# Optimization experiments

Measured on AMD Instinct MI355X. Metric: run time of the kernel, lower is better.

## Reference

```python
import jax, jax.numpy as jnp
import numpy as np

B = 8192          # num_envs
OPT = 16          # num options
SHARED = 22       # shared_state_size (hardcoded in module)
UNIQ = 8          # unique_state_size (hardcoded in module)
MIN_DUR, MAX_DUR = 0.1, 0.5  # const.gait_net.valid_swing_duration_range


def _w(k, o, i):
    return jax.random.normal(k, (o, i), jnp.float32) * (1.0 / np.sqrt(i))


def setup_inputs() -> dict:
    key = jax.random.key(0)
    ks = jax.random.split(key, 20)
    obs = jax.random.normal(ks[0], (B, SHARED + OPT * UNIQ), jnp.float32)
    flag = jax.random.uniform(ks[1], (B, OPT)) < 0.25
    u = obs[:, SHARED:].reshape(B, OPT, UNIQ)
    u = u.at[:, :, 0].set(jnp.where(flag, 1.0, u[:, :, 0]))
    obs = jnp.concatenate([obs[:, :SHARED], u.reshape(B, OPT * UNIQ)], axis=1)
    return {
        "obs": obs,
        "sw1": _w(ks[2], 256, 22), "sb1": jnp.zeros((256,), jnp.float32),
        "sw2": _w(ks[3], 256, 256), "sb2": jnp.zeros((256,), jnp.float32),
        "uw1": _w(ks[4], 128, 8), "ub1": jnp.zeros((128,), jnp.float32),
        "uw2": _w(ks[5], 128, 128), "ub2": jnp.zeros((128,), jnp.float32),
        "no_op_embedding": jax.random.normal(ks[6], (128,), jnp.float32),
        "tw1": _w(ks[7], 512, 384), "tb1": jnp.zeros((512,), jnp.float32),
        "tw2": _w(ks[8], 256, 512), "tb2": jnp.zeros((256,), jnp.float32),
        "vw": _w(ks[9], 1, 256), "vb": jnp.zeros((1,), jnp.float32),
        "dw": _w(ks[10], 1, 256), "db": jnp.zeros((1,), jnp.float32),
    }


def reference(obs, sw1, sb1, sw2, sb2, uw1, ub1, uw2, ub2, no_op_embedding,
              tw1, tb1, tw2, tb2, vw, vb, dw, db):
    relu = jax.nn.relu
    shared = obs[:, :SHARED]                               # [B, 22]
    uniq = obs[:, SHARED:].reshape(B, OPT, UNIQ)           # [B, OPT, 8]
    # shared encoder (22 -> 256 -> 256, relu output)
    se = relu(relu(shared @ sw1.T + sb1) @ sw2.T + sb2)    # [B, 256]
    # unique encoder applied to all options at once (8 -> 128 -> 128)
    ue = relu(relu(uniq @ uw1.T + ub1) @ uw2.T + ub2)      # [B, OPT, 128]
    no_op = uniq[:, :, 0] == 1.0                           # [B, OPT]
    ue = jnp.where(no_op[..., None], no_op_embedding, ue)
    trunk_in = jnp.concatenate(
        [jnp.broadcast_to(se[:, None, :], (B, OPT, se.shape[-1])), ue], axis=-1)
    t = relu(relu(trunk_in @ tw1.T + tb1) @ tw2.T + tb2)   # [B, OPT, 256]
    logits = (t @ vw.T + vb).squeeze(-1)                   # [B, OPT]
    duration = jax.nn.sigmoid((t @ dw.T + db).squeeze(-1)) * (MAX_DUR - MIN_DUR) + MIN_DUR
    return logits, duration
```

## Files before the change

kernel.cpp:

```cpp
#include <hip/hip_runtime.h>
#include <stdint.h>


static constexpr int B_ = 8192;

typedef __attribute__((ext_vector_type(8))) short bf16x8;
typedef __attribute__((ext_vector_type(4))) float f32x4;

__device__ __forceinline__ float u2f(uint16_t u) {
    union { uint32_t i; float f; } c; c.i = (uint32_t)u << 16; return c.f;
}
__device__ __forceinline__ uint16_t f2u(float f) {
    union { float f; uint32_t i; } c; c.f = f;
    uint32_t x = c.i;
    return (uint16_t)((x + 0x7FFFu + ((x >> 16) & 1u)) >> 16);
}

static constexpr size_t WCSE   = 0;
static constexpr size_t WTW1SE = 4194304;
static constexpr size_t WTW1UE = WTW1SE + 131072;
static constexpr size_t WTW2   = WTW1UE + 65536;
static constexpr size_t WUW2   = WTW2 + 131072;
static constexpr size_t WSW2   = WUW2 + 16384;
static constexpr size_t WUW1B  = WSW2 + 65536;

__global__ __launch_bounds__(256) void k_conv(
    const float* __restrict__ tw1, const float* __restrict__ tw2,
    const float* __restrict__ uw2, const float* __restrict__ sw2,
    const float* __restrict__ uw1, uint16_t* __restrict__ ws)
{
    int i4 = blockIdx.x * 256 + threadIdx.x;
    if (i4 >= 102400) {
        int q = i4 - 102400;
        int n = q >> 3, k0 = (q & 7) * 4;
        ushort4 o = {0, 0, 0, 0};
        if (k0 < 8) {
            float4 v = *reinterpret_cast<const float4*>(uw1 + n * 8 + k0);
            o.x = f2u(v.x); o.y = f2u(v.y); o.z = f2u(v.z); o.w = f2u(v.w);
        }
        *reinterpret_cast<ushort4*>(ws + WUW1B + n * 32 + k0) = o;
        return;
    }
    const float* src; size_t dst;
    if (i4 < 32768) {
        int g = i4 * 4, n = g >> 8, k = g & 255;
        src = tw1 + (size_t)n * 384 + k;
        dst = WTW1SE + (size_t)g;
    } else if (i4 < 49152) {
        int q = i4 - 32768, n = q >> 5, w = q & 31;
        src = tw1 + (size_t)n * 384 + 256 + w * 4;
        dst = WTW1UE + (size_t)n * 128 + w * 4;
    } else if (i4 < 81920) {
        int q = (i4 - 49152) * 4;
        src = tw2 + q; dst = WTW2 + q;
    } else if (i4 < 86016) {
        int q = (i4 - 81920) * 4;
        src = uw2 + q; dst = WUW2 + q;
    } else {
        int q = (i4 - 86016) * 4;
        src = sw2 + q; dst = WSW2 + q;
    }
    float4 v = *reinterpret_cast<const float4*>(src);
    ushort4 o;
    o.x = f2u(v.x); o.y = f2u(v.y); o.z = f2u(v.z); o.w = f2u(v.w);
    *reinterpret_cast<ushort4*>(ws + dst) = o;
}

__global__ __launch_bounds__(512) void k_cse(
    const float* __restrict__ obs,
    const float* __restrict__ sw1, const float* __restrict__ sb1,
    const float* __restrict__ sb2, const float* __restrict__ tb1,
    uint16_t* __restrict__ ws)
{
    __shared__ float xs[16][24];
    __shared__ uint16_t h1s[16 * 264];
    __shared__ uint16_t seL[16 * 264];
    const int t = threadIdx.x;
    const int b0 = blockIdx.x * 16;
    const uint16_t* sw2b   = ws + WSW2;
    const uint16_t* tw1seb = ws + WTW1SE;

    if (t < 352) {
        int e = t / 22, c = t - e * 22;
        xs[e][c] = obs[(size_t)(b0 + e) * 150 + c];
    }
    __syncthreads();
    {
        const int n = t & 255;
        float w[22];
        #pragma unroll
        for (int k = 0; k < 22; ++k) w[k] = sw1[n * 22 + k];
        const float bias = sb1[n];
        #pragma unroll
        for (int ii = 0; ii < 8; ++ii) {
            int e = (t >> 8) * 8 + ii;
            float a = bias;
            #pragma unroll
            for (int k = 0; k < 22; ++k) a += w[k] * xs[e][k];
            h1s[e * 264 + n] = f2u(fmaxf(a, 0.f));
        }
    }
    __syncthreads();
    const int wv = t >> 6, lane = t & 63, quad = lane >> 4, l16 = lane & 15;
    {
        f32x4 acc[2];
        #pragma unroll
        for (int nt = 0; nt < 2; ++nt) {
            float bv = sb2[wv * 32 + nt * 16 + l16];
            acc[nt] = {bv, bv, bv, bv};
        }
        const uint16_t* bb = sw2b + (size_t)(wv * 32 + l16) * 256 + quad * 8;
        bf16x8 bc[2], bn[2];
        bc[0] = *reinterpret_cast<const bf16x8*>(bb);
        bc[1] = *reinterpret_cast<const bf16x8*>(bb + 4096);
        #pragma unroll
        for (int kk = 0; kk < 8; ++kk) {
            if (kk < 7) {
                bn[0] = *reinterpret_cast<const bf16x8*>(bb + (kk + 1) * 32);
                bn[1] = *reinterpret_cast<const bf16x8*>(bb + 4096 + (kk + 1) * 32);
            }
            bf16x8 af = *reinterpret_cast<const bf16x8*>(
                &h1s[l16 * 264 + kk * 32 + quad * 8]);
            #pragma unroll
            for (int nt = 0; nt < 2; ++nt)
                acc[nt] = __builtin_amdgcn_mfma_f32_16x16x32_bf16(
                    af, bc[nt], acc[nt], 0, 0, 0);
            bc[0] = bn[0]; bc[1] = bn[1];
        }
        #pragma unroll
        for (int nt = 0; nt < 2; ++nt)
            #pragma unroll
            for (int r = 0; r < 4; ++r)
                seL[(quad * 4 + r) * 264 + wv * 32 + nt * 16 + l16] =
                    f2u(fmaxf(acc[nt][r], 0.f));
    }
    __syncthreads();
    {
        f32x4 acc[4];
        #pragma unroll
        for (int nt = 0; nt < 4; ++nt) {
            float bv = tb1[wv * 64 + nt * 16 + l16];
            acc[nt] = {bv, bv, bv, bv};
        }
        const uint16_t* bb = tw1seb + (size_t)(wv * 64 + l16) * 256 + quad * 8;
        bf16x8 bc[4], bn[4];
        #pragma unroll
        for (int nt = 0; nt < 4; ++nt)
            bc[nt] = *reinterpret_cast<const bf16x8*>(bb + nt * 4096);
        #pragma unroll
        for (int kk = 0; kk < 8; ++kk) {
            if (kk < 7) {
                #pragma unroll
                for (int nt = 0; nt < 4; ++nt)
                    bn[nt] = *reinterpret_cast<const bf16x8*>(
                        bb + nt * 4096 + (kk + 1) * 32);
            }
            bf16x8 af = *reinterpret_cast<const bf16x8*>(
                &seL[l16 * 264 + kk * 32 + quad * 8]);
            #pragma unroll
            for (int nt = 0; nt < 4; ++nt)
                acc[nt] = __builtin_amdgcn_mfma_f32_16x16x32_bf16(
                    af, bc[nt], acc[nt], 0, 0, 0);
            #pragma unroll
            for (int nt = 0; nt < 4; ++nt) bc[nt] = bn[nt];
        }
        #pragma unroll
        for (int nt = 0; nt < 4; ++nt)
            #pragma unroll
            for (int r = 0; r < 4; ++r)
                ws[WCSE + (size_t)(b0 + quad * 4 + r) * 512 +
                   wv * 64 + nt * 16 + l16] = f2u(acc[nt][r]);
    }
}

static constexpr int UQB_OFF  = 0;
static constexpr int NOOP_OFF = 5120;
static constexpr int CSE_OFF  = 5376;
static constexpr int H1U_OFF  = 9472;
static constexpr int UET_OFF  = 26880;
static constexpr int H1T_OFF  = 44288;
static constexpr int SMEM_SZ  = 78080;

__global__ __launch_bounds__(512, 4) void k_main(
    const float* __restrict__ obs,
    const float* __restrict__ ub1,
    const float* __restrict__ ub2, const float* __restrict__ emb,
    const float* __restrict__ tb2,
    const float* __restrict__ vw,  const float* __restrict__ vb,
    const float* __restrict__ dw,  const float* __restrict__ db,
    const uint16_t* __restrict__ wsb,
    float* __restrict__ out)
{
    __shared__ __align__(16) char smem[SMEM_SZ];
    uint16_t* uqb   = (uint16_t*)(smem + UQB_OFF);
    float*    noopf = (float*)(smem + NOOP_OFF);
    uint16_t* cseL  = (uint16_t*)(smem + CSE_OFF);
    uint16_t* h1u   = (uint16_t*)(smem + H1U_OFF);
    uint16_t* uet   = (uint16_t*)(smem + UET_OFF);
    uint16_t* h1t   = (uint16_t*)(smem + H1T_OFF);
    uint16_t* t2    = h1t;

    const int t    = threadIdx.x;
    const int wv   = t >> 6;
    const int lane = t & 63;
    const int quad = lane >> 4;
    const int l16  = lane & 15;
    const int b0   = blockIdx.x * 4;

    const uint16_t* csep  = wsb + WCSE;
    const uint16_t* tw1ue = wsb + WTW1UE;
    const uint16_t* tw2b  = wsb + WTW2;
    const uint16_t* uw2b  = wsb + WUW2;
    const uint16_t* uw1b  = wsb + WUW1B;

    {
        int r = t >> 3, q = t & 7;
        int e = r >> 4, o = r & 15;
        ushort4 ov = {0, 0, 0, 0};
        if (q < 2) {
            const float2* sp = reinterpret_cast<const float2*>(
                &obs[(size_t)(b0 + e) * 150 + 22 + o * 8 + q * 4]);
            float2 a = sp[0], b = sp[1];
            ov.x = f2u(a.x); ov.y = f2u(a.y); ov.z = f2u(b.x); ov.w = f2u(b.y);
        }
        *reinterpret_cast<ushort4*>(&uqb[r * 40 + q * 4]) = ov;
        #pragma unroll
        for (int ii = 0; ii < 2; ++ii) {
            int i = t + ii * 512;
            int ee = i >> 8, cc = i & 255;
            ((uint32_t*)cseL)[ee * 256 + cc] =
                ((const uint32_t*)(csep + (size_t)(b0 + ee) * 512))[cc];
        }
        if (t < 64) {
            int ee = t >> 4, oo = t & 15;
            noopf[t] = (obs[(size_t)(b0 + ee) * 150 + 22 + oo * 8] == 1.0f) ? 1.0f : 0.0f;
        }
    }
    __syncthreads();

    {
        const int n = wv * 16 + l16;
        const float bv = ub1[n];
        f32x4 acc[4];
        #pragma unroll
        for (int mt = 0; mt < 4; ++mt) acc[mt] = {bv, bv, bv, bv};
        bf16x8 bf = *reinterpret_cast<const bf16x8*>(&uw1b[n * 32 + quad * 8]);
        #pragma unroll
        for (int mt = 0; mt < 4; ++mt) {
            bf16x8 af = *reinterpret_cast<const bf16x8*>(
                &uqb[(mt * 16 + l16) * 40 + quad * 8]);
            acc[mt] = __builtin_amdgcn_mfma_f32_16x16x32_bf16(af, bf, acc[mt], 0, 0, 0);
        }
        #pragma unroll
        for (int mt = 0; mt < 4; ++mt)
            #pragma unroll
            for (int r = 0; r < 4; ++r) {
                int row = mt * 16 + quad * 4 + r;
                h1u[row * 136 + n] = f2u(fmaxf(acc[mt][r], 0.f));
            }
    }
    __syncthreads();

    {
        const int n = wv * 16 + l16;
        const float bv = ub2[n];
        const float ev = emb[n];
        f32x4 acc[4];
        #pragma unroll
        for (int mt = 0; mt < 4; ++mt) acc[mt] = {bv, bv, bv, bv};
        #pragma unroll
        for (int kk = 0; kk < 4; ++kk) {
            bf16x8 bf = *reinterpret_cast<const bf16x8*>(
                &uw2b[(size_t)n * 128 + kk * 32 + quad * 8]);
            #pragma unroll
            for (int mt = 0; mt < 4; ++mt) {
                bf16x8 af = *reinterpret_cast<const bf16x8*>(
                    &h1u[(mt * 16 + l16) * 136 + kk * 32 + quad * 8]);
                acc[mt] = __builtin_amdgcn_mfma_f32_16x16x32_bf16(af, bf, acc[mt], 0, 0, 0);
            }
        }
        #pragma unroll
        for (int mt = 0; mt < 4; ++mt)
            #pragma unroll
            for (int r = 0; r < 4; ++r) {
                int row = mt * 16 + quad * 4 + r;
                float v = (noopf[row] != 0.0f) ? ev : fmaxf(acc[mt][r], 0.f);
                uet[row * 136 + n] = f2u(v);
            }
    }
    __syncthreads();

    f32x4 acc2[4][2];
    #pragma unroll
    for (int nt = 0; nt < 2; ++nt) {
        float bv = tb2[wv * 32 + nt * 16 + l16];
        #pragma unroll
        for (int mt = 0; mt < 4; ++mt) acc2[mt][nt] = {bv, bv, bv, bv};
    }

    #pragma unroll
    for (int nc = 0; nc < 2; ++nc) {
        {
            f32x4 acc1[4][2];
            #pragma unroll
            for (int nt = 0; nt < 2; ++nt) {
                int n = nc * 256 + wv * 32 + nt * 16 + l16;
                #pragma unroll
                for (int mt = 0; mt < 4; ++mt) {
                    float v = u2f(cseL[mt * 512 + n]);
                    acc1[mt][nt] = {v, v, v, v};
                }
            }
            const uint16_t* bb = tw1ue + (size_t)(nc * 256 + wv * 32 + l16) * 128
                                 + quad * 8;
            bf16x8 bc[2], bn[2];
            bc[0] = *reinterpret_cast<const bf16x8*>(bb);
            bc[1] = *reinterpret_cast<const bf16x8*>(bb + 2048);
            #pragma unroll
            for (int kk = 0; kk < 4; ++kk) {
                if (kk < 3) {
                    bn[0] = *reinterpret_cast<const bf16x8*>(bb + (kk + 1) * 32);
                    bn[1] = *reinterpret_cast<const bf16x8*>(bb + 2048 + (kk + 1) * 32);
                }
                bf16x8 af[4];
                #pragma unroll
                for (int mt = 0; mt < 4; ++mt)
                    af[mt] = *reinterpret_cast<const bf16x8*>(
                        &uet[(mt * 16 + l16) * 136 + kk * 32 + quad * 8]);
                #pragma unroll
                for (int mt = 0; mt < 4; ++mt)
                    #pragma unroll
                    for (int nt = 0; nt < 2; ++nt)
                        acc1[mt][nt] = __builtin_amdgcn_mfma_f32_16x16x32_bf16(
                            af[mt], bc[nt], acc1[mt][nt], 0, 0, 0);
                bc[0] = bn[0]; bc[1] = bn[1];
            }
            #pragma unroll
            for (int mt = 0; mt < 4; ++mt)
                #pragma unroll
                for (int nt = 0; nt < 2; ++nt)
                    #pragma unroll
                    for (int r = 0; r < 4; ++r) {
                        int row = mt * 16 + quad * 4 + r;
                        h1t[row * 264 + wv * 32 + nt * 16 + l16] =
                            f2u(fmaxf(acc1[mt][nt][r], 0.f));
                    }
        }
        __syncthreads();
        {
            const uint16_t* cb = tw2b + (size_t)(wv * 32 + l16) * 512 + nc * 256
                                 + quad * 8;
            bf16x8 cc[2], cn[2];
            cc[0] = *reinterpret_cast<const bf16x8*>(cb);
            cc[1] = *reinterpret_cast<const bf16x8*>(cb + 8192);
            #pragma unroll
            for (int k2 = 0; k2 < 8; ++k2) {
                if (k2 < 7) {
                    cn[0] = *reinterpret_cast<const bf16x8*>(cb + (k2 + 1) * 32);
                    cn[1] = *reinterpret_cast<const bf16x8*>(cb + 8192 + (k2 + 1) * 32);
                }
                bf16x8 af[4];
                #pragma unroll
                for (int mt = 0; mt < 4; ++mt)
                    af[mt] = *reinterpret_cast<const bf16x8*>(
                        &h1t[(mt * 16 + l16) * 264 + k2 * 32 + quad * 8]);
                #pragma unroll
                for (int mt = 0; mt < 4; ++mt)
                    #pragma unroll
                    for (int nt = 0; nt < 2; ++nt)
                        acc2[mt][nt] = __builtin_amdgcn_mfma_f32_16x16x32_bf16(
                            af[mt], cc[nt], acc2[mt][nt], 0, 0, 0);
                cc[0] = cn[0]; cc[1] = cn[1];
            }
        }
        if (nc == 0) __syncthreads();
    }
    __syncthreads();
    #pragma unroll
    for (int mt = 0; mt < 4; ++mt)
        #pragma unroll
        for (int nt = 0; nt < 2; ++nt)
            #pragma unroll
            for (int r = 0; r < 4; ++r) {
                int row = mt * 16 + quad * 4 + r;
                t2[row * 264 + wv * 32 + nt * 16 + l16] =
                    f2u(fmaxf(acc2[mt][nt][r], 0.f));
            }
    __syncthreads();

    {
        float vwf[4], dwf[4];
        #pragma unroll
        for (int j = 0; j < 4; ++j) {
            vwf[j] = vw[lane + 64 * j];
            dwf[j] = dw[lane + 64 * j];
        }
        const float vbf = vb[0], dbf = db[0];
        #pragma unroll
        for (int rr = 0; rr < 8; ++rr) {
            int row = wv * 8 + rr;
            float sv = 0.f, sd = 0.f;
            #pragma unroll
            for (int j = 0; j < 4; ++j) {
                float tv = u2f(t2[row * 264 + lane + 64 * j]);
                sv += tv * vwf[j];
                sd += tv * dwf[j];
            }
            #pragma unroll
            for (int off = 32; off > 0; off >>= 1) {
                sv += __shfl_down(sv, off);
                sd += __shfl_down(sd, off);
            }
            if (lane == 0) {
                int g = blockIdx.x * 64 + row;
                out[g] = sv + vbf;
                float z = sd + dbf;
                float sig = 1.f / (1.f + __expf(-z));
                out[B_ * 16 + g] = sig * 0.4f + 0.1f;
            }
        }
    }
}

extern "C" void kernel_launch(void* const* d_in, const int* in_sizes, int n_in,
                              void* d_out, int out_size, void* d_ws, size_t ws_size,
                              hipStream_t stream) {
    const float* obs = (const float*)d_in[0];
    const float* sw1 = (const float*)d_in[1];
    const float* sb1 = (const float*)d_in[2];
    const float* sw2 = (const float*)d_in[3];
    const float* sb2 = (const float*)d_in[4];
    const float* uw1 = (const float*)d_in[5];
    const float* ub1 = (const float*)d_in[6];
    const float* uw2 = (const float*)d_in[7];
    const float* ub2 = (const float*)d_in[8];
    const float* emb = (const float*)d_in[9];
    const float* tw1 = (const float*)d_in[10];
    const float* tb1 = (const float*)d_in[11];
    const float* tw2 = (const float*)d_in[12];
    const float* tb2 = (const float*)d_in[13];
    const float* vw  = (const float*)d_in[14];
    const float* vb  = (const float*)d_in[15];
    const float* dw  = (const float*)d_in[16];
    const float* db  = (const float*)d_in[17];

    uint16_t* wsb = (uint16_t*)d_ws;

    k_conv<<<404, 256, 0, stream>>>(tw1, tw2, uw2, sw2, uw1, wsb);
    k_cse<<<512, 512, 0, stream>>>(obs, sw1, sb1, sb2, tb1, wsb);
    k_main<<<B_ / 4, 512, 0, stream>>>(obs, ub1, ub2, emb, tb2,
                                       vw, vb, dw, db, wsb, (float*)d_out);
}
```

Baseline: 239.3 us.

## Fuse shared-encoder kernel into main kernel, keep per-env trunk contribution in LDS

Removes the separate k_cse launch. Each k_main block now computes the shared encoder (22->256->256) and its tw1 contribution for its own 4 environments, writing the result straight into LDS instead of round-tripping a 512-wide bf16 vector per env through global workspace. This saves one kernel launch and the global write/read of the precomputed shared contribution. The cost is that the MFMA tiles use 16 rows where only 4 are valid, so most of that shared-encoder compute is wasted, and every block reloads the sw2/tw1se weights.

```diff
diff --git a/kernel.cpp b/kernel.cpp
--- a/kernel.cpp
+++ b/kernel.cpp
@@ -66,123 +66,21 @@
     *reinterpret_cast<ushort4*>(ws + dst) = o;
 }
 
-__global__ __launch_bounds__(512) void k_cse(
-    const float* __restrict__ obs,
-    const float* __restrict__ sw1, const float* __restrict__ sb1,
-    const float* __restrict__ sb2, const float* __restrict__ tb1,
-    uint16_t* __restrict__ ws)
-{
-    __shared__ float xs[16][24];
-    __shared__ uint16_t h1s[16 * 264];
-    __shared__ uint16_t seL[16 * 264];
-    const int t = threadIdx.x;
-    const int b0 = blockIdx.x * 16;
-    const uint16_t* sw2b   = ws + WSW2;
-    const uint16_t* tw1seb = ws + WTW1SE;
-
-    if (t < 352) {
-        int e = t / 22, c = t - e * 22;
-        xs[e][c] = obs[(size_t)(b0 + e) * 150 + c];
-    }
-    __syncthreads();
-    {
-        const int n = t & 255;
-        float w[22];
-        #pragma unroll
-        for (int k = 0; k < 22; ++k) w[k] = sw1[n * 22 + k];
-        const float bias = sb1[n];
-        #pragma unroll
-        for (int ii = 0; ii < 8; ++ii) {
-            int e = (t >> 8) * 8 + ii;
-            float a = bias;
-            #pragma unroll
-            for (int k = 0; k < 22; ++k) a += w[k] * xs[e][k];
-            h1s[e * 264 + n] = f2u(fmaxf(a, 0.f));
-        }
-    }
-    __syncthreads();
-    const int wv = t >> 6, lane = t & 63, quad = lane >> 4, l16 = lane & 15;
-    {
-        f32x4 acc[2];
-        #pragma unroll
-        for (int nt = 0; nt < 2; ++nt) {
-            float bv = sb2[wv * 32 + nt * 16 + l16];
-            acc[nt] = {bv, bv, bv, bv};
-        }
-        const uint16_t* bb = sw2b + (size_t)(wv * 32 + l16) * 256 + quad * 8;
-        bf16x8 bc[2], bn[2];
-        bc[0] = *reinterpret_cast<const bf16x8*>(bb);
-        bc[1] = *reinterpret_cast<const bf16x8*>(bb + 4096);
-        #pragma unroll
-        for (int kk = 0; kk < 8; ++kk) {
-            if (kk < 7) {
-                bn[0] = *reinterpret_cast<const bf16x8*>(bb + (kk + 1) * 32);
-                bn[1] = *reinterpret_cast<const bf16x8*>(bb + 4096 + (kk + 1) * 32);
-            }
-            bf16x8 af = *reinterpret_cast<const bf16x8*>(
-                &h1s[l16 * 264 + kk * 32 + quad * 8]);
-            #pragma unroll
-            for (int nt = 0; nt < 2; ++nt)
-                acc[nt] = __builtin_amdgcn_mfma_f32_16x16x32_bf16(
-                    af, bc[nt], acc[nt], 0, 0, 0);
-            bc[0] = bn[0]; bc[1] = bn[1];
-        }
-        #pragma unroll
-        for (int nt = 0; nt < 2; ++nt)
-            #pragma unroll
-            for (int r = 0; r < 4; ++r)
-                seL[(quad * 4 + r) * 264 + wv * 32 + nt * 16 + l16] =
-                    f2u(fmaxf(acc[nt][r], 0.f));
-    }
-    __syncthreads();
-    {
-        f32x4 acc[4];
-        #pragma unroll
-        for (int nt = 0; nt < 4; ++nt) {
-            float bv = tb1[wv * 64 + nt * 16 + l16];
-            acc[nt] = {bv, bv, bv, bv};
-        }
-        const uint16_t* bb = tw1seb + (size_t)(wv * 64 + l16) * 256 + quad * 8;
-        bf16x8 bc[4], bn[4];
-        #pragma unroll
-        for (int nt = 0; nt < 4; ++nt)
-            bc[nt] = *reinterpret_cast<const bf16x8*>(bb + nt * 4096);
-        #pragma unroll
-        for (int kk = 0; kk < 8; ++kk) {
-            if (kk < 7) {
-                #pragma unroll
-                for (int nt = 0; nt < 4; ++nt)
-                    bn[nt] = *reinterpret_cast<const bf16x8*>(
-                        bb + nt * 4096 + (kk + 1) * 32);
-            }
-            bf16x8 af = *reinterpret_cast<const bf16x8*>(
-                &seL[l16 * 264 + kk * 32 + quad * 8]);
-            #pragma unroll
-            for (int nt = 0; nt < 4; ++nt)
-                acc[nt] = __builtin_amdgcn_mfma_f32_16x16x32_bf16(
-                    af, bc[nt], acc[nt], 0, 0, 0);
-            #pragma unroll
-            for (int nt = 0; nt < 4; ++nt) bc[nt] = bn[nt];
-        }
-        #pragma unroll
-        for (int nt = 0; nt < 4; ++nt)
-            #pragma unroll
-            for (int r = 0; r < 4; ++r)
-                ws[WCSE + (size_t)(b0 + quad * 4 + r) * 512 +
-                   wv * 64 + nt * 16 + l16] = f2u(acc[nt][r]);
-    }
-}
-
 static constexpr int UQB_OFF  = 0;
 static constexpr int NOOP_OFF = 5120;
 static constexpr int CSE_OFF  = 5376;
 static constexpr int H1U_OFF  = 9472;
 static constexpr int UET_OFF  = 26880;
 static constexpr int H1T_OFF  = 44288;
+static constexpr int SEH1_OFF = H1T_OFF;
+static constexpr int SEL_OFF  = H1T_OFF + 8448;
+static constexpr int XS_OFF   = H1T_OFF + 16896;
 static constexpr int SMEM_SZ  = 78080;
 
 __global__ __launch_bounds__(512, 4) void k_main(
     const float* __restrict__ obs,
+    const float* __restrict__ sw1, const float* __restrict__ sb1,
+    const float* __restrict__ sb2, const float* __restrict__ tb1,
     const float* __restrict__ ub1,
     const float* __restrict__ ub2, const float* __restrict__ emb,
     const float* __restrict__ tb2,
@@ -199,6 +97,9 @@
     uint16_t* uet   = (uint16_t*)(smem + UET_OFF);
     uint16_t* h1t   = (uint16_t*)(smem + H1T_OFF);
     uint16_t* t2    = h1t;
+    uint16_t* h1s   = (uint16_t*)(smem + SEH1_OFF);
+    uint16_t* seL   = (uint16_t*)(smem + SEL_OFF);
+    float*    xs    = (float*)(smem + XS_OFF);
 
     const int t    = threadIdx.x;
     const int wv   = t >> 6;
@@ -207,11 +108,12 @@
     const int l16  = lane & 15;
     const int b0   = blockIdx.x * 4;
 
-    const uint16_t* csep  = wsb + WCSE;
-    const uint16_t* tw1ue = wsb + WTW1UE;
-    const uint16_t* tw2b  = wsb + WTW2;
-    const uint16_t* uw2b  = wsb + WUW2;
-    const uint16_t* uw1b  = wsb + WUW1B;
+    const uint16_t* tw1ue  = wsb + WTW1UE;
+    const uint16_t* tw2b   = wsb + WTW2;
+    const uint16_t* uw2b   = wsb + WUW2;
+    const uint16_t* uw1b   = wsb + WUW1B;
+    const uint16_t* sw2b   = wsb + WSW2;
+    const uint16_t* tw1seb = wsb + WTW1SE;
 
     {
         int r = t >> 3, q = t & 7;
@@ -224,16 +126,103 @@
             ov.x = f2u(a.x); ov.y = f2u(a.y); ov.z = f2u(b.x); ov.w = f2u(b.y);
         }
         *reinterpret_cast<ushort4*>(&uqb[r * 40 + q * 4]) = ov;
-        #pragma unroll
-        for (int ii = 0; ii < 2; ++ii) {
-            int i = t + ii * 512;
-            int ee = i >> 8, cc = i & 255;
-            ((uint32_t*)cseL)[ee * 256 + cc] =
-                ((const uint32_t*)(csep + (size_t)(b0 + ee) * 512))[cc];
+        if (t < 88) {
+            int e2 = t / 22, c = t - e2 * 22;
+            xs[e2 * 24 + c] = obs[(size_t)(b0 + e2) * 150 + c];
         }
         if (t < 64) {
             int ee = t >> 4, oo = t & 15;
             noopf[t] = (obs[(size_t)(b0 + ee) * 150 + 22 + oo * 8] == 1.0f) ? 1.0f : 0.0f;
+        }
+    }
+    __syncthreads();
+
+    {
+        const int n = t & 255;
+        float w[22];
+        #pragma unroll
+        for (int k = 0; k < 22; ++k) w[k] = sw1[n * 22 + k];
+        const float bias = sb1[n];
+        #pragma unroll
+        for (int ii = 0; ii < 2; ++ii) {
+            int e = (t >> 8) * 2 + ii;
+            float a = bias;
+            #pragma unroll
+            for (int k = 0; k < 22; ++k) a += w[k] * xs[e * 24 + k];
+            h1s[e * 264 + n] = f2u(fmaxf(a, 0.f));
+        }
+    }
+    __syncthreads();
+
+    {
+        f32x4 acc[2];
+        #pragma unroll
+        for (int nt = 0; nt < 2; ++nt) {
+            float bv = sb2[wv * 32 + nt * 16 + l16];
+            acc[nt] = {bv, bv, bv, bv};
+        }
+        const uint16_t* bb = sw2b + (size_t)(wv * 32 + l16) * 256 + quad * 8;
+        bf16x8 bc[2], bn[2];
+        bc[0] = *reinterpret_cast<const bf16x8*>(bb);
+        bc[1] = *reinterpret_cast<const bf16x8*>(bb + 4096);
+        #pragma unroll
+        for (int kk = 0; kk < 8; ++kk) {
+            if (kk < 7) {
+                bn[0] = *reinterpret_cast<const bf16x8*>(bb + (kk + 1) * 32);
+                bn[1] = *reinterpret_cast<const bf16x8*>(bb + 4096 + (kk + 1) * 32);
+            }
+            bf16x8 af = *reinterpret_cast<const bf16x8*>(
+                &h1s[l16 * 264 + kk * 32 + quad * 8]);
+            #pragma unroll
+            for (int nt = 0; nt < 2; ++nt)
+                acc[nt] = __builtin_amdgcn_mfma_f32_16x16x32_bf16(
+                    af, bc[nt], acc[nt], 0, 0, 0);
+            bc[0] = bn[0]; bc[1] = bn[1];
+        }
+        #pragma unroll
+        for (int nt = 0; nt < 2; ++nt)
+            #pragma unroll
+            for (int r = 0; r < 4; ++r)
+                seL[(quad * 4 + r) * 264 + wv * 32 + nt * 16 + l16] =
+                    f2u(fmaxf(acc[nt][r], 0.f));
+    }
+    __syncthreads();
+
+    {
+        f32x4 acc[4];
+        #pragma unroll
+        for (int nt = 0; nt < 4; ++nt) {
+            float bv = tb1[wv * 64 + nt * 16 + l16];
+            acc[nt] = {bv, bv, bv, bv};
+        }
+        const uint16_t* bb = tw1seb + (size_t)(wv * 64 + l16) * 256 + quad * 8;
+        bf16x8 bc[4], bn[4];
+        #pragma unroll
+        for (int nt = 0; nt < 4; ++nt)
+            bc[nt] = *reinterpret_cast<const bf16x8*>(bb + nt * 4096);
+        #pragma unroll
+        for (int kk = 0; kk < 8; ++kk) {
+            if (kk < 7) {
+                #pragma unroll
+                for (int nt = 0; nt < 4; ++nt)
+                    bn[nt] = *reinterpret_cast<const bf16x8*>(
+                        bb + nt * 4096 + (kk + 1) * 32);
+            }
+            bf16x8 af = *reinterpret_cast<const bf16x8*>(
+                &seL[l16 * 264 + kk * 32 + quad * 8]);
+            #pragma unroll
+            for (int nt = 0; nt < 4; ++nt)
+                acc[nt] = __builtin_amdgcn_mfma_f32_16x16x32_bf16(
+                    af, bc[nt], acc[nt], 0, 0, 0);
+            #pragma unroll
+            for (int nt = 0; nt < 4; ++nt) bc[nt] = bn[nt];
+        }
+        if (quad == 0) {
+            #pragma unroll
+            for (int nt = 0; nt < 4; ++nt)
+                #pragma unroll
+                for (int r = 0; r < 4; ++r)
+                    cseL[r * 512 + wv * 64 + nt * 16 + l16] = f2u(acc[nt][r]);
         }
     }
     __syncthreads();
@@ -447,7 +436,7 @@
     uint16_t* wsb = (uint16_t*)d_ws;
 
     k_conv<<<404, 256, 0, stream>>>(tw1, tw2, uw2, sw2, uw1, wsb);
-    k_cse<<<512, 512, 0, stream>>>(obs, sw1, sb1, sb2, tb1, wsb);
-    k_main<<<B_ / 4, 512, 0, stream>>>(obs, ub1, ub2, emb, tb2,
+    k_main<<<B_ / 4, 512, 0, stream>>>(obs, sw1, sb1, sb2, tb1,
+                                       ub1, ub2, emb, tb2,
                                        vw, vb, dw, db, wsb, (float*)d_out);
 }
```

Measured after the change: 288.4 us. 20.5% more time.
